# Optimization experiments

Measured on AMD Instinct MI355X. Metric: run time of the kernel, lower is better.

Reference implementation:

```python
import jax, jax.numpy as jnp
import numpy as np

B, F_IN, HID, H, S = 256, 1024, 1024, 16, 128
TEMP = float((HID // H) ** 0.5)  # 8.0


def setup_inputs() -> dict:
    key = jax.random.key(0)
    ks = jax.random.split(key, 7)
    return {
        "x": jax.random.normal(ks[0], (B, F_IN, S), dtype=jnp.float32),
        "Wq": jax.random.normal(ks[1], (HID, F_IN), dtype=jnp.float32) * (1.0 / np.sqrt(F_IN)),
        "bq": jax.random.normal(ks[2], (HID,), dtype=jnp.float32) * 0.01,
        "Wk": jax.random.normal(ks[3], (HID, F_IN), dtype=jnp.float32) * (1.0 / np.sqrt(F_IN)),
        "bk": jax.random.normal(ks[4], (HID,), dtype=jnp.float32) * 0.01,
        "Wo": jax.random.normal(ks[5], (S,), dtype=jnp.float32) * (1.0 / np.sqrt(S)),
        "bo": jax.random.normal(ks[6], (1,), dtype=jnp.float32) * 0.01,
    }


def _to_heads(t):
    # (B, F, S) -> (B, H, S, F//H), matching reshape(B,H,F/H,S).permute(0,1,3,2)
    b, f, s = t.shape
    return t.reshape(b, H, f // H, s).transpose(0, 1, 3, 2)


def reference(x, Wq, bq, Wk, bk, Wo, bo):
    # 1x1 Conv1d == per-position linear over channel dim
    q = jnp.einsum('bis,hi->bhs', x, Wq) + bq[None, :, None]
    k = jnp.einsum('bis,hi->bhs', x, Wk) + bk[None, :, None]
    qh = _to_heads(q)          # (B,H,S,HID/H)
    kh = _to_heads(k)          # (B,H,S,HID/H)
    vh = _to_heads(x)          # (B,H,S,F_IN/H)  -- v is the raw input, unprojected
    scores = jnp.einsum('bhsd,bhtd->bhst', qh, kh) / TEMP
    attn = jax.nn.softmax(scores, axis=-1)
    out = jnp.einsum('bhst,bhtd->bhsd', attn, vh)   # (B,H,S,F_IN/H)
    # _reshape_from_batches: (B,H,S,dv) -> (B, F_IN, S)
    out = out.transpose(0, 1, 3, 2).reshape(x.shape[0], F_IN, S)
    # map_o: Linear(num_users, 1) over last axis, then squeeze
    score = jnp.einsum('bfs,s->bf', out, Wo) + bo[0]
    return score
```

## Files before the change

### kernel.cpp

```cpp
#include <hip/hip_runtime.h>

#define F 1024
#define S 128
#define H 16
#define D 64
#define CK 64
#define NCHUNK 16

typedef short bf16x8 __attribute__((ext_vector_type(8)));
typedef float f32x4  __attribute__((ext_vector_type(4)));

#define XS_UNITS ((size_t)128 * NCHUNK * 2048)
#define WB_UNITS ((size_t)8 * NCHUNK * 2048)
#define WS_NEED ((XS_UNITS + WB_UNITS) * 16)

#define MAIN_LDS_BYTES (8192 * 16 + 8 * 128 * 4 + 128 * 4)

__device__ __forceinline__ unsigned short f2bf(float f) {
    unsigned u = __float_as_uint(f);
    u += 0x7fffu + ((u >> 16) & 1u);
    return (unsigned short)(u >> 16);
}

__device__ __forceinline__ uint4 pack8(const float* f) {
    uint4 u;
    u.x = (unsigned)f2bf(f[0]) | ((unsigned)f2bf(f[1]) << 16);
    u.y = (unsigned)f2bf(f[2]) | ((unsigned)f2bf(f[3]) << 16);
    u.z = (unsigned)f2bf(f[4]) | ((unsigned)f2bf(f[5]) << 16);
    u.w = (unsigned)f2bf(f[6]) | ((unsigned)f2bf(f[7]) << 16);
    return u;
}

typedef __attribute__((address_space(1))) const unsigned int as1_u32;
typedef __attribute__((address_space(3))) unsigned int as3_u32;

__device__ __forceinline__ void async_cp16(const uint4* g, uint4* l) {
    __builtin_amdgcn_global_load_lds((as1_u32*)g, (as3_u32*)l, 16, 0, 0);
}

__device__ __forceinline__ void bar()   { __builtin_amdgcn_s_barrier(); }
__device__ __forceinline__ void sb0()   { __builtin_amdgcn_sched_barrier(0); }

template<int N> __device__ __forceinline__ void lgkm() {
    asm volatile("s_waitcnt lgkmcnt(%0)" :: "n"(N));
}
template<int N> __device__ __forceinline__ void vmw() {
    asm volatile("s_waitcnt vmcnt(%0)" :: "n"(N));
}

__global__ void prep(const float* __restrict__ x,
                     const float* __restrict__ Wq,
                     const float* __restrict__ Wk,
                     uint4* __restrict__ xs,
                     uint4* __restrict__ wb)
{
    const int tid = threadIdx.x;
    const int blk = blockIdx.x;
    if (blk < 4096) {
        const int b = blk >> 4, ch = blk & 15;
        const float* xb = x + ((size_t)b * F + ch * CK) * S;
        uint4* dst = xs + ((size_t)(b >> 1) * NCHUNK + ch) * 2048 + (b & 1) * 128;
#pragma unroll
        for (int j = 0; j < 4; ++j) {
            const int u  = tid + j * 256;
            const int kc = u >> 7;
            const int s  = u & 127;
            const float* rp = xb + (size_t)(kc * 8) * S + s;
            float f[8];
#pragma unroll
            for (int jj = 0; jj < 8; ++jj) f[jj] = rp[jj * S];
            dst[kc * 256 + s] = pack8(f);
        }
    } else {
        const int blk2 = blk - 4096;
        const int h = blk2 >> 4, ch = blk2 & 15;
        uint4* dst = wb + ((size_t)(h >> 1) * NCHUNK + ch) * 2048 + (h & 1) * 128;
#pragma unroll
        for (int j = 0; j < 4; ++j) {
            const int u  = tid + j * 256;
            const int kc = u >> 7;
            const int m  = u & 127;
            const float* srcp = (m < 64)
                ? (Wq + (size_t)(h * D + m) * F + ch * CK + kc * 8)
                : (Wk + (size_t)(h * D + m - 64) * F + ch * CK + kc * 8);
            float f[8];
            float4 a = ((const float4*)srcp)[0];
            float4 c = ((const float4*)srcp)[1];
            f[0] = a.x; f[1] = a.y; f[2] = a.z; f[3] = a.w;
            f[4] = c.x; f[5] = c.y; f[6] = c.z; f[7] = c.w;
            dst[kc * 256 + m] = pack8(f);
        }
    }
}

__device__ __forceinline__ void read4(const uint4* mat, int base, bf16x8 (&r)[4]) {
    r[0] = *(const bf16x8*)&mat[base];
    r[1] = *(const bf16x8*)&mat[base + 16];
    r[2] = *(const bf16x8*)&mat[base + 32];
    r[3] = *(const bf16x8*)&mat[base + 48];
}

template<int RB>
__device__ __forceinline__ void mfma16(f32x4 (&acc)[8][4], const bf16x8 (&af)[4], const bf16x8 (&br)[4]) {
#pragma unroll
    for (int mt = 0; mt < 4; ++mt)
#pragma unroll
        for (int nt = 0; nt < 4; ++nt)
            acc[RB + mt][nt] = __builtin_amdgcn_mfma_f32_16x16x32_bf16(af[mt], br[nt], acc[RB + mt][nt], 0, 0, 0);
}

template<int HALF>
__device__ __forceinline__ void stage_half(uint4* mat, const uint4* wbase, const uint4* xbase,
                                           int tgt, int wv, int lane) {
    const int bufb = (tgt & 1) * 4096;
    const uint4* g;
    int l;
    if constexpr (HALF == 0)      { g = wbase + (size_t)tgt * 2048;        l = bufb;        }
    else if constexpr (HALF == 1) { g = xbase + (size_t)tgt * 2048;        l = bufb + 2048; }
    else if constexpr (HALF == 2) { g = wbase + (size_t)tgt * 2048 + 1024; l = bufb + 1024; }
    else                          { g = xbase + (size_t)tgt * 2048 + 1024; l = bufb + 3072; }
    async_cp16(g + wv * 128 + lane,      &mat[l + wv * 128]);
    async_cp16(g + wv * 128 + 64 + lane, &mat[l + wv * 128 + 64]);
}

template<int CUR, int SMODE>
__device__ __forceinline__ void ktile2(uint4* mat, const uint4* wbase, const uint4* xbase,
                                       int t, int wv, int lane, int wm, int wn, int q, int l15,
                                       f32x4 (&acc)[8][4])
{
    const int ab = CUR * 4096 + wm * 128 + l15 + q * 256;
    const int bb = CUR * 4096 + 2048 + wn * 64 + l15 + q * 256;
    {
        bf16x8 a0[4], a1[4], b0[4];
        read4(mat, ab, a0);
        read4(mat, bb, b0);
        read4(mat, ab + 64, a1);
        sb0();
        if constexpr (SMODE >= 1) stage_half<2>(mat, wbase, xbase, t + 1, wv, lane);
        sb0();
        lgkm<4>(); sb0();
        __builtin_amdgcn_s_setprio(1); mfma16<0>(acc, a0, b0); __builtin_amdgcn_s_setprio(0); sb0();
        if constexpr (SMODE >= 1) stage_half<3>(mat, wbase, xbase, t + 1, wv, lane);
        sb0();
        lgkm<0>(); sb0();
        __builtin_amdgcn_s_setprio(1); mfma16<4>(acc, a1, b0); __builtin_amdgcn_s_setprio(0); sb0();
    }
    if constexpr (SMODE >= 1) { vmw<4>(); } else { vmw<0>(); }
    bar(); sb0();
    {
        bf16x8 a2[4], a3[4], b1[4];
        read4(mat, ab + 1024, a2);
        read4(mat, bb + 1024, b1);
        read4(mat, ab + 1024 + 64, a3);
        sb0();
        if constexpr (SMODE == 2) stage_half<0>(mat, wbase, xbase, t + 2, wv, lane);
        sb0();
        lgkm<4>(); sb0();
        __builtin_amdgcn_s_setprio(1); mfma16<0>(acc, a2, b1); __builtin_amdgcn_s_setprio(0); sb0();
        if constexpr (SMODE == 2) stage_half<1>(mat, wbase, xbase, t + 2, wv, lane);
        sb0();
        lgkm<0>(); sb0();
        __builtin_amdgcn_s_setprio(1); mfma16<4>(acc, a3, b1); __builtin_amdgcn_s_setprio(0); sb0();
    }
    bar(); sb0();
}

__launch_bounds__(512, 2)
__global__ void attn_main(const float* __restrict__ x,
                          const uint4* __restrict__ xs,
                          const uint4* __restrict__ wb,
                          const float* __restrict__ bq,
                          const float* __restrict__ bk,
                          const float* __restrict__ Wo,
                          const float* __restrict__ bo,
                          float* __restrict__ out)
{
    (void)x;
    extern __shared__ char smraw[];
    uint4* mat   = (uint4*)smraw;
    float* wpart = (float*)(smraw + 8192 * 16);

    const int tid  = threadIdx.x;
    const int lane = tid & 63;
    const int wv   = tid >> 6;
    const int l15  = lane & 15;
    const int q    = lane >> 4;
    const int wm   = wv >> 2;
    const int wn   = wv & 3;

    const int g    = blockIdx.x;
    const int xcd  = g & 7;
    const int slot = g >> 3;
    const int bg   = xcd * 16 + (slot & 15);
    const int hg   = slot >> 4;

    const uint4* wbase = wb + (size_t)hg * NCHUNK * 2048;
    const uint4* xbase = xs + (size_t)bg * NCHUNK * 2048;

    f32x4 acc[8][4];
#pragma unroll
    for (int mi = 0; mi < 8; ++mi)
#pragma unroll
        for (int ni = 0; ni < 4; ++ni) acc[mi][ni] = (f32x4){0.f, 0.f, 0.f, 0.f};

    stage_half<0>(mat, wbase, xbase, 0, wv, lane);
    stage_half<1>(mat, wbase, xbase, 0, wv, lane);
    stage_half<2>(mat, wbase, xbase, 0, wv, lane);
    stage_half<3>(mat, wbase, xbase, 0, wv, lane);
    stage_half<0>(mat, wbase, xbase, 1, wv, lane);
    stage_half<1>(mat, wbase, xbase, 1, wv, lane);
    vmw<4>();
    bar(); sb0();

#pragma unroll 1
    for (int i = 0; i < 7; ++i) {
        ktile2<0, 2>(mat, wbase, xbase, 2 * i,     wv, lane, wm, wn, q, l15, acc);
        ktile2<1, 2>(mat, wbase, xbase, 2 * i + 1, wv, lane, wm, wn, q, l15, acc);
    }
    ktile2<0, 1>(mat, wbase, xbase, 14, wv, lane, wm, wn, q, l15, acc);
    ktile2<1, 0>(mat, wbase, xbase, 15, wv, lane, wm, wn, q, l15, acc);

    __syncthreads();

    {
        unsigned short* m16 = (unsigned short*)mat;
        const int hglobw = hg * 2 + wm;
#pragma unroll
        for (int rt = 0; rt < 8; ++rt) {
            const int mh0   = rt * 16 + q * 4;
            const int d0    = mh0 & 63;
            const int kbase = (mh0 < 64) ? 0 : 1024;
            float bias4[4];
#pragma unroll
            for (int rr = 0; rr < 4; ++rr)
                bias4[rr] = (mh0 < 64) ? bq[hglobw * D + d0 + rr] : bk[hglobw * D + d0 + rr];
#pragma unroll
            for (int ct = 0; ct < 4; ++ct) {
                const int col = wn * 64 + ct * 16 + l15;
                const int bj  = col >> 7;
                const int s   = col & 127;
                const int c   = wm * 2 + bj;
                unsigned long long pv = 0;
#pragma unroll
                for (int rr = 0; rr < 4; ++rr)
                    pv |= (unsigned long long)f2bf(acc[rt][ct][rr] + bias4[rr]) << (16 * rr);
                const int unit = c * 2048 + kbase + s * 8 + ((d0 >> 3) ^ (s & 7));
                *(unsigned long long*)&m16[unit * 8 + (d0 & 7)] = pv;
            }
        }
    }
    __syncthreads();

    const int ce   = ((wv >> 2) << 1) | ((wv >> 1) & 1);
    const int half = wv & 1;
    const int qb = ce * 2048;
    const int kb = ce * 2048 + 1024;
    const int bglob = bg * 2 + (ce & 1);
    const int hglob = hg * 2 + (ce >> 1);

    f32x4 p[4][8];
#pragma unroll
    for (int mt = 0; mt < 4; ++mt)
#pragma unroll
        for (int nt = 0; nt < 8; ++nt) p[mt][nt] = (f32x4){0.f, 0.f, 0.f, 0.f};
#pragma unroll
    for (int ks = 0; ks < 2; ++ks) {
        const int kcq = ks * 4 + q;
        bf16x8 a2[4], b2[8];
#pragma unroll
        for (int mt = 0; mt < 4; ++mt) {
            const int row = half * 64 + mt * 16 + l15;
            a2[mt] = *(const bf16x8*)&mat[qb + row * 8 + (kcq ^ (row & 7))];
        }
#pragma unroll
        for (int nt = 0; nt < 8; ++nt) {
            const int trow = nt * 16 + l15;
            b2[nt] = *(const bf16x8*)&mat[kb + trow * 8 + (kcq ^ (trow & 7))];
        }
#pragma unroll
        for (int mt = 0; mt < 4; ++mt)
#pragma unroll
            for (int nt = 0; nt < 8; ++nt)
                p[mt][nt] = __builtin_amdgcn_mfma_f32_16x16x32_bf16(a2[mt], b2[nt], p[mt][nt], 0, 0, 0);
    }

    const int ell = half * 64 + lane;
    const int kc5 = ell >> 4;
    const int sg5 = ell & 15;
    const uint4* xsrc = xbase + (size_t)hglob * 2048 + kc5 * 256 + (ce & 1) * 128 + sg5 * 8;
    uint4 xu[8];
#pragma unroll
    for (int jj = 0; jj < 8; ++jj) xu[jj] = xsrc[jj];

    float pw[8];
#pragma unroll
    for (int nt = 0; nt < 8; ++nt) pw[nt] = 0.f;
#pragma unroll
    for (int mt = 0; mt < 4; ++mt) {
#pragma unroll
        for (int rr = 0; rr < 4; ++rr) {
            const int srow = half * 64 + mt * 16 + q * 4 + rr;
            float e[8];
            float l = 0.f;
#pragma unroll
            for (int nt = 0; nt < 8; ++nt) {
                e[nt] = __expf(fminf(p[mt][nt][rr] * 0.125f, 80.f));
                l += e[nt];
            }
#pragma unroll
            for (int off = 1; off < 16; off <<= 1) l += __shfl_xor(l, off);
            const float cw = Wo[srow] / l;
#pragma unroll
            for (int nt = 0; nt < 8; ++nt) pw[nt] = fmaf(cw, e[nt], pw[nt]);
        }
    }
#pragma unroll
    for (int nt = 0; nt < 8; ++nt) {
        pw[nt] += __shfl_xor(pw[nt], 16);
        pw[nt] += __shfl_xor(pw[nt], 32);
    }
    if (q == 0) {
#pragma unroll
        for (int nt = 0; nt < 8; ++nt) wpart[wv * 128 + nt * 16 + l15] = pw[nt];
    }
    __syncthreads();

    {
        const float* w0 = wpart + 2 * ce * 128;
        const float* w1 = w0 + 128;
        float acc8[8];
#pragma unroll
        for (int e = 0; e < 8; ++e) acc8[e] = 0.f;
#pragma unroll
        for (int jj = 0; jj < 8; ++jj) {
            const int s = sg5 * 8 + jj;
            const float w = w0[s] + w1[s];
            const unsigned* du = (const unsigned*)&xu[jj];
#pragma unroll
            for (int dw = 0; dw < 4; ++dw) {
                const unsigned v = du[dw];
                acc8[dw * 2 + 0] = fmaf(__uint_as_float(v << 16), w, acc8[dw * 2 + 0]);
                acc8[dw * 2 + 1] = fmaf(__uint_as_float(v & 0xffff0000u), w, acc8[dw * 2 + 1]);
            }
        }
#pragma unroll
        for (int e = 0; e < 8; ++e) {
#pragma unroll
            for (int off = 1; off < 16; off <<= 1)
                acc8[e] += __shfl_xor(acc8[e], off);
        }
        if (sg5 < 8)
            out[(size_t)bglob * F + hglob * D + kc5 * 8 + sg5] = acc8[sg5] + bo[0];
    }
}

struct SmemT {
    uint4 mat[2048];
    float wpart[4][S];
    float wfin[S];
};

__launch_bounds__(256, 4)
__global__ void attn_fallback(const float* __restrict__ x,
                              const float* __restrict__ Wq,
                              const float* __restrict__ bq,
                              const float* __restrict__ Wk,
                              const float* __restrict__ bk,
                              const float* __restrict__ Wo,
                              const float* __restrict__ bo,
                              float* __restrict__ out)
{
    __shared__ SmemT sm;
    const int tid  = threadIdx.x;
    const int lane = tid & 63;
    const int wv   = tid >> 6;
    const int l15  = lane & 15;
    const int q    = lane >> 4;

    const int g    = blockIdx.x;
    const int xcd  = g & 7;
    const int slot = g >> 3;
    const int hg   = slot >> 7;
    const int r0   = slot & 127;
    const int b    = xcd * 32 + (r0 >> 2);
    const int h    = hg * 4 + (r0 & 3);

    const float* xb  = x  + (size_t)b * (F * S);
    const float* wqh = Wq + (size_t)h * D * F;
    const float* wkh = Wk + (size_t)h * D * F;

    const int m0 = (wv & 1) * 64;
    const int n0 = (wv >> 1) * 64;

    f32x4 acc[4][4];
#pragma unroll
    for (int mt = 0; mt < 4; ++mt)
#pragma unroll
        for (int nt = 0; nt < 4; ++nt) acc[mt][nt] = (f32x4){0.f, 0.f, 0.f, 0.f};

    const int mq  = tid >> 2;
    const int kq  = tid & 3;
    const int s0x = (tid & 63) * 2;
    const int iq  = tid >> 6;

    for (int ch = 0; ch < NCHUNK; ++ch) {
        const int c0 = ch * CK;
        __syncthreads();
        {
            const int key = mq & 7;
            float f[16];
            const float4* srcq = (const float4*)(wqh + (size_t)mq * F + (c0 + kq * 16));
#pragma unroll
            for (int j = 0; j < 4; ++j) {
                float4 v = srcq[j];
                f[4*j] = v.x; f[4*j+1] = v.y; f[4*j+2] = v.z; f[4*j+3] = v.w;
            }
            sm.mat[mq * 8 + ((kq * 2    ) ^ key)] = pack8(f);
            sm.mat[mq * 8 + ((kq * 2 + 1) ^ key)] = pack8(f + 8);
            const float4* srck = (const float4*)(wkh + (size_t)mq * F + (c0 + kq * 16));
#pragma unroll
            for (int j = 0; j < 4; ++j) {
                float4 v = srck[j];
                f[4*j] = v.x; f[4*j+1] = v.y; f[4*j+2] = v.z; f[4*j+3] = v.w;
            }
            sm.mat[(64 + mq) * 8 + ((kq * 2    ) ^ key)] = pack8(f);
            sm.mat[(64 + mq) * 8 + ((kq * 2 + 1) ^ key)] = pack8(f + 8);
        }
        {
            const float* src = xb + (size_t)(c0 + iq * 16) * S + s0x;
            float fa[8], fb[8];
#pragma unroll
            for (int grp = 0; grp < 2; ++grp) {
#pragma unroll
                for (int j = 0; j < 8; ++j) {
                    float2 v = *(const float2*)(src + (size_t)(grp * 8 + j) * S);
                    fa[j] = v.x; fb[j] = v.y;
                }
                const int kc = iq * 2 + grp;
                sm.mat[1024 + (s0x    ) * 8 + (kc ^ ((s0x    ) & 7))] = pack8(fa);
                sm.mat[1024 + (s0x + 1) * 8 + (kc ^ ((s0x + 1) & 7))] = pack8(fb);
            }
        }
        __syncthreads();
#pragma unroll
        for (int ks = 0; ks < 2; ++ks) {
            bf16x8 af[4], br[4];
#pragma unroll
            for (int mt = 0; mt < 4; ++mt) {
                const int row = m0 + mt * 16 + l15;
                af[mt] = *(const bf16x8*)&sm.mat[row * 8 + ((ks * 4 + q) ^ (row & 7))];
            }
#pragma unroll
            for (int nt = 0; nt < 4; ++nt) {
                const int row = n0 + nt * 16 + l15;
                br[nt] = *(const bf16x8*)&sm.mat[1024 + row * 8 + ((ks * 4 + q) ^ (row & 7))];
            }
#pragma unroll
            for (int mt = 0; mt < 4; ++mt)
#pragma unroll
                for (int nt = 0; nt < 4; ++nt)
                    acc[mt][nt] = __builtin_amdgcn_mfma_f32_16x16x32_bf16(
                        af[mt], br[nt], acc[mt][nt], 0, 0, 0);
        }
    }

    __syncthreads();
    {
        unsigned short* m16 = (unsigned short*)sm.mat;
#pragma unroll
        for (int mt = 0; mt < 4; ++mt) {
#pragma unroll
            for (int rr = 0; rr < 4; ++rr) {
                const int m = m0 + mt * 16 + q * 4 + rr;
                const int d = m & 63;
                const float bias = (m < 64) ? bq[h * D + d] : bk[h * D + d];
                const int base = (m < 64) ? 0 : 8192;
#pragma unroll
                for (int nt = 0; nt < 4; ++nt) {
                    const int s = n0 + nt * 16 + l15;
                    const float v = acc[mt][nt][rr] + bias;
                    const int unit = s * 8 + (((d >> 3)) ^ (s & 7));
                    m16[base + unit * 8 + (d & 7)] = f2bf(v);
                }
            }
        }
    }
    __syncthreads();

    f32x4 p[2][8];
#pragma unroll
    for (int mt = 0; mt < 2; ++mt)
#pragma unroll
        for (int nt = 0; nt < 8; ++nt) p[mt][nt] = (f32x4){0.f, 0.f, 0.f, 0.f};

#pragma unroll
    for (int ks = 0; ks < 2; ++ks) {
        bf16x8 a2[2], b2[8];
#pragma unroll
        for (int mt = 0; mt < 2; ++mt) {
            const int row = wv * 32 + mt * 16 + l15;
            a2[mt] = *(const bf16x8*)&sm.mat[row * 8 + ((ks * 4 + q) ^ (row & 7))];
        }
#pragma unroll
        for (int nt = 0; nt < 8; ++nt) {
            const int row = nt * 16 + l15;
            b2[nt] = *(const bf16x8*)&sm.mat[1024 + row * 8 + ((ks * 4 + q) ^ (row & 7))];
        }
#pragma unroll
        for (int mt = 0; mt < 2; ++mt)
#pragma unroll
            for (int nt = 0; nt < 8; ++nt)
                p[mt][nt] = __builtin_amdgcn_mfma_f32_16x16x32_bf16(a2[mt], b2[nt], p[mt][nt], 0, 0, 0);
    }

    float pw[8];
#pragma unroll
    for (int nt = 0; nt < 8; ++nt) pw[nt] = 0.f;

#pragma unroll
    for (int mt = 0; mt < 2; ++mt) {
#pragma unroll
        for (int rr = 0; rr < 4; ++rr) {
            const int srow = wv * 32 + mt * 16 + q * 4 + rr;
            float mx = p[mt][0][rr];
#pragma unroll
            for (int nt = 1; nt < 8; ++nt) mx = fmaxf(mx, p[mt][nt][rr]);
#pragma unroll
            for (int off = 1; off < 16; off <<= 1) mx = fmaxf(mx, __shfl_xor(mx, off));
            float e[8];
            float l = 0.f;
#pragma unroll
            for (int nt = 0; nt < 8; ++nt) {
                e[nt] = __expf((p[mt][nt][rr] - mx) * 0.125f);
                l += e[nt];
            }
#pragma unroll
            for (int off = 1; off < 16; off <<= 1) l += __shfl_xor(l, off);
            const float c = Wo[srow] / l;
#pragma unroll
            for (int nt = 0; nt < 8; ++nt) pw[nt] = fmaf(c, e[nt], pw[nt]);
        }
    }
#pragma unroll
    for (int nt = 0; nt < 8; ++nt) {
        pw[nt] += __shfl_xor(pw[nt], 16);
        pw[nt] += __shfl_xor(pw[nt], 32);
    }
    if (q == 0) {
#pragma unroll
        for (int nt = 0; nt < 8; ++nt) sm.wpart[wv][nt * 16 + l15] = pw[nt];
    }
    __syncthreads();
    if (tid < S)
        sm.wfin[tid] = sm.wpart[0][tid] + sm.wpart[1][tid] + sm.wpart[2][tid] + sm.wpart[3][tid];
    __syncthreads();

    {
        const int dd   = tid >> 2;
        const int part = tid & 3;
        const float* xv = xb + (size_t)(h * D + dd) * S + part * 32;
        float a5 = 0.f;
#pragma unroll 8
        for (int t = 0; t < 32; ++t) a5 = fmaf(sm.wfin[part * 32 + t], xv[t], a5);
        a5 += __shfl_xor(a5, 1);
        a5 += __shfl_xor(a5, 2);
        if (part == 0) out[(size_t)b * F + h * D + dd] = a5 + bo[0];
    }
}

extern "C" void kernel_launch(void* const* d_in, const int* in_sizes, int n_in,
                              void* d_out, int out_size, void* d_ws, size_t ws_size,
                              hipStream_t stream) {
    const float* x  = (const float*)d_in[0];
    const float* Wq = (const float*)d_in[1];
    const float* bq = (const float*)d_in[2];
    const float* Wk = (const float*)d_in[3];
    const float* bk = (const float*)d_in[4];
    const float* Wo = (const float*)d_in[5];
    const float* bo = (const float*)d_in[6];
    float* out = (float*)d_out;

    if (ws_size >= WS_NEED) {
        uint4* xsp = (uint4*)d_ws;
        uint4* wbp = (uint4*)((char*)d_ws + XS_UNITS * 16);
        static bool attr_done = false;
        if (!attr_done) {
            (void)hipFuncSetAttribute(reinterpret_cast<const void*>(attn_main),
                                      hipFuncAttributeMaxDynamicSharedMemorySize, MAIN_LDS_BYTES);
            attr_done = true;
        }
        prep<<<dim3(4096 + 256), dim3(256), 0, stream>>>(x, Wq, Wk, xsp, wbp);
        attn_main<<<dim3(1024), dim3(512), MAIN_LDS_BYTES, stream>>>(x, xsp, wbp, bq, bk, Wo, bo, out);
    } else {
        attn_fallback<<<dim3(256 * H), dim3(256), 0, stream>>>(x, Wq, bq, Wk, bk, Wo, bo, out);
    }
}
```

Baseline: 342.1 us.

## Switch GEMM mainloop to triple-buffered 32-wide K tiles with one barrier each

The projection GEMM mainloop moves from double-buffered 64-wide K tiles, staged in two halves with two barriers and interleaved LDS waits per tile, to a three-slot ring of 32-wide K tiles. Each tile loads all A/B fragments, issues async global-to-LDS copies for tile t+2, runs 32 MFMAs, then waits on the tile t+1 copies and hits a single barrier. The goal is fewer barriers and less fine-grained wait/issue interleaving, with a deeper prefetch distance to hide global latency. In exchange there are twice as many K iterations, and it drops the explicit lgkm waits that let MFMAs start while later LDS reads were still in flight. It also holds more fragment registers live per tile, which could hurt scheduling under the 2-blocks-per-CU launch bound.

```diff
diff --git a/kernel.cpp b/kernel.cpp
--- a/kernel.cpp
+++ b/kernel.cpp
@@ -4,7 +4,6 @@
 #define S 128
 #define H 16
 #define D 64
-#define CK 64
 #define NCHUNK 16
 
 typedef short bf16x8 __attribute__((ext_vector_type(8)));
@@ -41,9 +40,6 @@
 __device__ __forceinline__ void bar()   { __builtin_amdgcn_s_barrier(); }
 __device__ __forceinline__ void sb0()   { __builtin_amdgcn_sched_barrier(0); }
 
-template<int N> __device__ __forceinline__ void lgkm() {
-    asm volatile("s_waitcnt lgkmcnt(%0)" :: "n"(N));
-}
 template<int N> __device__ __forceinline__ void vmw() {
     asm volatile("s_waitcnt vmcnt(%0)" :: "n"(N));
 }
@@ -58,7 +54,7 @@
     const int blk = blockIdx.x;
     if (blk < 4096) {
         const int b = blk >> 4, ch = blk & 15;
-        const float* xb = x + ((size_t)b * F + ch * CK) * S;
+        const float* xb = x + ((size_t)b * F + ch * 64) * S;
         uint4* dst = xs + ((size_t)(b >> 1) * NCHUNK + ch) * 2048 + (b & 1) * 128;
 #pragma unroll
         for (int j = 0; j < 4; ++j) {
@@ -81,8 +77,8 @@
             const int kc = u >> 7;
             const int m  = u & 127;
             const float* srcp = (m < 64)
-                ? (Wq + (size_t)(h * D + m) * F + ch * CK + kc * 8)
-                : (Wk + (size_t)(h * D + m - 64) * F + ch * CK + kc * 8);
+                ? (Wq + (size_t)(h * D + m) * F + ch * 64 + kc * 8)
+                : (Wk + (size_t)(h * D + m - 64) * F + ch * 64 + kc * 8);
             float f[8];
             float4 a = ((const float4*)srcp)[0];
             float4 c = ((const float4*)srcp)[1];
@@ -93,76 +89,44 @@
     }
 }
 
-__device__ __forceinline__ void read4(const uint4* mat, int base, bf16x8 (&r)[4]) {
-    r[0] = *(const bf16x8*)&mat[base];
-    r[1] = *(const bf16x8*)&mat[base + 16];
-    r[2] = *(const bf16x8*)&mat[base + 32];
-    r[3] = *(const bf16x8*)&mat[base + 48];
-}
-
-template<int RB>
-__device__ __forceinline__ void mfma16(f32x4 (&acc)[8][4], const bf16x8 (&af)[4], const bf16x8 (&br)[4]) {
-#pragma unroll
-    for (int mt = 0; mt < 4; ++mt)
-#pragma unroll
-        for (int nt = 0; nt < 4; ++nt)
-            acc[RB + mt][nt] = __builtin_amdgcn_mfma_f32_16x16x32_bf16(af[mt], br[nt], acc[RB + mt][nt], 0, 0, 0);
-}
-
-template<int HALF>
-__device__ __forceinline__ void stage_half(uint4* mat, const uint4* wbase, const uint4* xbase,
-                                           int tgt, int wv, int lane) {
-    const int bufb = (tgt & 1) * 4096;
-    const uint4* g;
-    int l;
-    if constexpr (HALF == 0)      { g = wbase + (size_t)tgt * 2048;        l = bufb;        }
-    else if constexpr (HALF == 1) { g = xbase + (size_t)tgt * 2048;        l = bufb + 2048; }
-    else if constexpr (HALF == 2) { g = wbase + (size_t)tgt * 2048 + 1024; l = bufb + 1024; }
-    else                          { g = xbase + (size_t)tgt * 2048 + 1024; l = bufb + 3072; }
-    async_cp16(g + wv * 128 + lane,      &mat[l + wv * 128]);
-    async_cp16(g + wv * 128 + 64 + lane, &mat[l + wv * 128 + 64]);
-}
-
-template<int CUR, int SMODE>
-__device__ __forceinline__ void ktile2(uint4* mat, const uint4* wbase, const uint4* xbase,
+template<int BUF>
+__device__ __forceinline__ void stage32(uint4* mat, const uint4* wbase, const uint4* xbase,
+                                        int t, int wv, int lane) {
+    uint4* la = mat + BUF * 2048 + wv * 128;
+    const uint4* ga = wbase + (size_t)t * 1024 + wv * 128;
+    async_cp16(ga + lane,      la);
+    async_cp16(ga + 64 + lane, la + 64);
+    uint4* lb = mat + BUF * 2048 + 1024 + wv * 128;
+    const uint4* gb = xbase + (size_t)t * 1024 + wv * 128;
+    async_cp16(gb + lane,      lb);
+    async_cp16(gb + 64 + lane, lb + 64);
+}
+
+template<int CUR, int SMODE, int WEND>
+__device__ __forceinline__ void ktile3(uint4* mat, const uint4* wbase, const uint4* xbase,
                                        int t, int wv, int lane, int wm, int wn, int q, int l15,
                                        f32x4 (&acc)[8][4])
 {
-    const int ab = CUR * 4096 + wm * 128 + l15 + q * 256;
-    const int bb = CUR * 4096 + 2048 + wn * 64 + l15 + q * 256;
-    {
-        bf16x8 a0[4], a1[4], b0[4];
-        read4(mat, ab, a0);
-        read4(mat, bb, b0);
-        read4(mat, ab + 64, a1);
-        sb0();
-        if constexpr (SMODE >= 1) stage_half<2>(mat, wbase, xbase, t + 1, wv, lane);
-        sb0();
-        lgkm<4>(); sb0();
-        __builtin_amdgcn_s_setprio(1); mfma16<0>(acc, a0, b0); __builtin_amdgcn_s_setprio(0); sb0();
-        if constexpr (SMODE >= 1) stage_half<3>(mat, wbase, xbase, t + 1, wv, lane);
-        sb0();
-        lgkm<0>(); sb0();
-        __builtin_amdgcn_s_setprio(1); mfma16<4>(acc, a1, b0); __builtin_amdgcn_s_setprio(0); sb0();
-    }
-    if constexpr (SMODE >= 1) { vmw<4>(); } else { vmw<0>(); }
-    bar(); sb0();
-    {
-        bf16x8 a2[4], a3[4], b1[4];
-        read4(mat, ab + 1024, a2);
-        read4(mat, bb + 1024, b1);
-        read4(mat, ab + 1024 + 64, a3);
-        sb0();
-        if constexpr (SMODE == 2) stage_half<0>(mat, wbase, xbase, t + 2, wv, lane);
-        sb0();
-        lgkm<4>(); sb0();
-        __builtin_amdgcn_s_setprio(1); mfma16<0>(acc, a2, b1); __builtin_amdgcn_s_setprio(0); sb0();
-        if constexpr (SMODE == 2) stage_half<1>(mat, wbase, xbase, t + 2, wv, lane);
-        sb0();
-        lgkm<0>(); sb0();
-        __builtin_amdgcn_s_setprio(1); mfma16<4>(acc, a3, b1); __builtin_amdgcn_s_setprio(0); sb0();
-    }
-    bar(); sb0();
+    constexpr int NXT = (CUR + 2) % 3;
+    const int ab = CUR * 2048 + q * 256 + wm * 128 + l15;
+    const int bb = CUR * 2048 + 1024 + q * 256 + wn * 64 + l15;
+    bf16x8 b[4], a[8];
+#pragma unroll
+    for (int j = 0; j < 4; ++j) b[j] = *(const bf16x8*)&mat[bb + j * 16];
+#pragma unroll
+    for (int i = 0; i < 8; ++i) a[i] = *(const bf16x8*)&mat[ab + i * 16];
+    if constexpr (SMODE) stage32<NXT>(mat, wbase, xbase, t + 2, wv, lane);
+    sb0();
+    __builtin_amdgcn_s_setprio(1);
+#pragma unroll
+    for (int i = 0; i < 8; ++i)
+#pragma unroll
+        for (int j = 0; j < 4; ++j)
+            acc[i][j] = __builtin_amdgcn_mfma_f32_16x16x32_bf16(a[i], b[j], acc[i][j], 0, 0, 0);
+    __builtin_amdgcn_s_setprio(0);
+    sb0();
+    if constexpr (WEND == 4)      { vmw<4>(); bar(); sb0(); }
+    else if constexpr (WEND == 0) { vmw<0>(); bar(); sb0(); }
 }
 
 __launch_bounds__(512, 2)
@@ -203,22 +167,19 @@
 #pragma unroll
         for (int ni = 0; ni < 4; ++ni) acc[mi][ni] = (f32x4){0.f, 0.f, 0.f, 0.f};
 
-    stage_half<0>(mat, wbase, xbase, 0, wv, lane);
-    stage_half<1>(mat, wbase, xbase, 0, wv, lane);
-    stage_half<2>(mat, wbase, xbase, 0, wv, lane);
-    stage_half<3>(mat, wbase, xbase, 0, wv, lane);
-    stage_half<0>(mat, wbase, xbase, 1, wv, lane);
-    stage_half<1>(mat, wbase, xbase, 1, wv, lane);
+    stage32<0>(mat, wbase, xbase, 0, wv, lane);
+    stage32<1>(mat, wbase, xbase, 1, wv, lane);
     vmw<4>();
     bar(); sb0();
 
 #pragma unroll 1
-    for (int i = 0; i < 7; ++i) {
-        ktile2<0, 2>(mat, wbase, xbase, 2 * i,     wv, lane, wm, wn, q, l15, acc);
-        ktile2<1, 2>(mat, wbase, xbase, 2 * i + 1, wv, lane, wm, wn, q, l15, acc);
-    }
-    ktile2<0, 1>(mat, wbase, xbase, 14, wv, lane, wm, wn, q, l15, acc);
-    ktile2<1, 0>(mat, wbase, xbase, 15, wv, lane, wm, wn, q, l15, acc);
+    for (int i = 0; i < 10; ++i) {
+        ktile3<0, 1, 4>(mat, wbase, xbase, 3 * i,     wv, lane, wm, wn, q, l15, acc);
+        ktile3<1, 1, 4>(mat, wbase, xbase, 3 * i + 1, wv, lane, wm, wn, q, l15, acc);
+        ktile3<2, 1, 4>(mat, wbase, xbase, 3 * i + 2, wv, lane, wm, wn, q, l15, acc);
+    }
+    ktile3<0, 0, 0>(mat, wbase, xbase, 30, wv, lane, wm, wn, q, l15, acc);
+    ktile3<1, 0, -1>(mat, wbase, xbase, 31, wv, lane, wm, wn, q, l15, acc);
 
     __syncthreads();
 
@@ -404,7 +365,7 @@
     const int iq  = tid >> 6;
 
     for (int ch = 0; ch < NCHUNK; ++ch) {
-        const int c0 = ch * CK;
+        const int c0 = ch * 64;
         __syncthreads();
         {
             const int key = mq & 7;
```

Measured after the change: 355.5 us. +3.9%, slower.
